# Optimization experiments

Measured on AMD Instinct MI355X. Metric: run time of the kernel, lower is better.

The kernel has to match this reference:

```python
import jax, jax.numpy as jnp
import numpy as np
from jax import lax

T, B, A_DIM, Z_DIM, K_MIX, HID = 128, 256, 16, 32, 8, 128
Q_REG = 1e-3
R_REG = 1e-3


def setup_inputs() -> dict:
    key = jax.random.key(0)
    ks = jax.random.split(key, 16)
    s = 1.0 / np.sqrt(HID)
    reg = 0.9
    as_ = jax.random.normal(ks[0], (T, B, A_DIM), dtype=jnp.float32)
    mat_A_K = (1.0 - reg) * jax.random.normal(ks[1], (K_MIX, Z_DIM, Z_DIM)) + reg * jnp.eye(Z_DIM)
    mat_C_K = (1.0 - reg) * jax.random.normal(ks[2], (K_MIX, A_DIM, Z_DIM)) + reg * jnp.eye(A_DIM, Z_DIM)
    # Cholesky factors of near-identity SPD matrices (as in torch init)
    Q_L = jnp.tril(0.05 * jax.random.normal(ks[3], (Z_DIM, Z_DIM))) + jnp.eye(Z_DIM)
    R_L = jnp.tril(0.05 * jax.random.normal(ks[4], (A_DIM, A_DIM))) + jnp.eye(A_DIM)
    init_mean = jnp.zeros((Z_DIM,), dtype=jnp.float32)
    init_cov = jnp.eye(Z_DIM, dtype=jnp.float32)
    u = lambda k, shp: jax.random.uniform(k, shp, minval=-s, maxval=s, dtype=jnp.float32)
    return dict(
        as_=as_, mat_A_K=mat_A_K, mat_C_K=mat_C_K, Q_L=Q_L, R_L=R_L,
        init_mean=init_mean, init_cov=init_cov,
        W_ih0=u(ks[5], (4 * HID, A_DIM)), W_hh0=u(ks[6], (4 * HID, HID)),
        b_ih0=u(ks[7], (4 * HID,)), b_hh0=u(ks[8], (4 * HID,)),
        W_ih1=u(ks[9], (4 * HID, HID)), W_hh1=u(ks[10], (4 * HID, HID)),
        b_ih1=u(ks[11], (4 * HID,)), b_hh1=u(ks[12], (4 * HID,)),
        W_out=u(ks[13], (K_MIX, HID)), b_out=u(ks[14], (K_MIX,)),
    )


def _lstm_cell(x, h, c, W_ih, W_hh, b_ih, b_hh):
    g = x @ W_ih.T + b_ih + h @ W_hh.T + b_hh
    i, f, gg, o = jnp.split(g, 4, axis=-1)
    c2 = jax.nn.sigmoid(f) * c + jax.nn.sigmoid(i) * jnp.tanh(gg)
    h2 = jax.nn.sigmoid(o) * jnp.tanh(c2)
    return h2, c2


def reference(as_, mat_A_K, mat_C_K, Q_L, R_L, init_mean, init_cov,
              W_ih0, W_hh0, b_ih0, b_hh0, W_ih1, W_hh1, b_ih1, b_hh1,
              W_out, b_out):
    Tn, Bn, a_dim = as_.shape
    Kn, z_dim, _ = mat_A_K.shape
    Hn = W_hh0.shape[1]
    Q = Q_L @ Q_L.T + Q_REG * jnp.eye(z_dim, dtype=as_.dtype)
    R = R_L @ R_L.T + R_REG * jnp.eye(a_dim, dtype=as_.dtype)

    def weight_model(a, h0, c0, h1, c1):
        h0, c0 = _lstm_cell(a, h0, c0, W_ih0, W_hh0, b_ih0, b_hh0)
        h1, c1 = _lstm_cell(h0, h1, c1, W_ih1, W_hh1, b_ih1, b_hh1)
        w = jax.nn.softmax(h1 @ W_out.T + b_out, axis=-1)
        return w, h0, c0, h1, c1

    def step(carry, a_t):
        mean_p, cov_p, weight, h0, c0, h1, c1 = carry
        # mixture matrices for this step (weight == previous step's w_next; ones at t=0)
        mat_A = jnp.einsum('bk,kij->bij', weight, mat_A_K)
        mat_C = jnp.einsum('bk,kij->bij', weight, mat_C_K)
        # sample_control = ('mean','mean'), observation_mask=None -> a = as_[t]
        w_next, h0, c0, h1, c1 = weight_model(a_t, h0, c0, h1, c1)
        mat_A_next = jnp.einsum('bk,kij->bij', w_next, mat_A_K)
        CP = mat_C @ cov_p                                   # (B,a,z)
        S = CP @ jnp.swapaxes(mat_C, 1, 2) + R               # (B,a,a)
        K_t = cov_p @ jnp.swapaxes(mat_C, 1, 2) @ jnp.linalg.inv(S)
        mean_t = mean_p + K_t @ (a_t[..., None] - mat_C @ mean_p)
        mean_p2 = mat_A_next @ mean_t
        cov_t = cov_p - K_t @ CP
        cov_t = 0.5 * (cov_t + jnp.swapaxes(cov_t, 1, 2))
        cov_p2 = mat_A_next @ cov_t @ jnp.swapaxes(mat_A_next, 1, 2) + Q
        cov_p2 = 0.5 * (cov_p2 + jnp.swapaxes(cov_p2, 1, 2))
        new_carry = (mean_p2, cov_p2, w_next, h0, c0, h1, c1)
        outs = (mean_t, cov_t, mean_p2, cov_p2, mat_A, mat_C, a_t)
        return new_carry, outs

    init = (
        jnp.broadcast_to(init_mean[None, :, None], (Bn, z_dim, 1)),
        jnp.broadcast_to(init_cov[None], (Bn, z_dim, z_dim)),
        jnp.ones((Bn, Kn), dtype=as_.dtype),
        jnp.zeros((Bn, Hn), dtype=as_.dtype), jnp.zeros((Bn, Hn), dtype=as_.dtype),
        jnp.zeros((Bn, Hn), dtype=as_.dtype), jnp.zeros((Bn, Hn), dtype=as_.dtype),
    )
    carry, ys = lax.scan(step, init, as_)
    means, covs, next_means, next_covs, mat_As, mat_Cs, a_seq = ys
    w_fin = carry[2]
    mat_A_fin = jnp.einsum('bk,kij->bij', w_fin, mat_A_K)
    mat_C_fin = jnp.einsum('bk,kij->bij', w_fin, mat_C_K)
    mat_As = jnp.concatenate([mat_As, mat_A_fin[None]], axis=0)   # (T+1,B,z,z)
    mat_Cs = jnp.concatenate([mat_Cs, mat_C_fin[None]], axis=0)   # (T+1,B,a,z)
    a_out = a_seq[:, None]                                        # (T,1,B,a) as in torch stack
    return means, covs, next_means, next_covs, mat_As, mat_Cs, a_out
```

## Files before the change

### kernel.cpp

```cpp
#include <hip/hip_runtime.h>
#include <hip/hip_fp16.h>
#include <math.h>

#define T_STEPS 128
#define B_SZ 256
#define AD 16
#define ZD 32
#define KM 8
#define HID 128
#define G4H 512
#define NTHR 512

#define WS_WQ   0
#define WS_WI0  98304
#define WS_BS0  102400
#define WS_BS1  102912
#define WS_Q    103424
#define WS_R    104448

typedef float f32x4 __attribute__((ext_vector_type(4)));

__device__ __forceinline__ unsigned pk16(float lo, float hi) {
  unsigned a = __half_as_ushort(__float2half_rn(lo));
  unsigned b = __half_as_ushort(__float2half_rn(hi));
  return a | (b << 16);
}

__global__ void ssm_prep_kernel(const float* __restrict__ Wih0, const float* __restrict__ Whh0,
                                const float* __restrict__ Wih1, const float* __restrict__ Whh1,
                                const float* __restrict__ bih0, const float* __restrict__ bhh0,
                                const float* __restrict__ bih1, const float* __restrict__ bhh1,
                                const float* __restrict__ QL, const float* __restrict__ RL,
                                float* __restrict__ ws) {
  unsigned* wsu = (unsigned*)ws;
  int tid = blockIdx.x * blockDim.x + threadIdx.x;
  int nt = gridDim.x * blockDim.x;
  for (int j = tid; j < G4H; j += nt) {
    for (int d4 = 0; d4 < 48; ++d4) {
      for (int m = 0; m < 4; ++m) {
        int dd = (d4 & 15) * 4 + m;
        const float* src = (d4 < 16) ? Whh0 : (d4 < 32) ? Wih1 : Whh1;
        wsu[WS_WQ + (d4 * 512 + j) * 4 + m] =
            pk16(src[j * 128 + 2 * dd], src[j * 128 + 2 * dd + 1]);
      }
    }
    for (int k = 0; k < 8; ++k)
      wsu[WS_WI0 + k * 512 + j] = pk16(Wih0[j * 16 + 2 * k], Wih0[j * 16 + 2 * k + 1]);
    ws[WS_BS0 + j] = bih0[j] + bhh0[j];
    ws[WS_BS1 + j] = bih1[j] + bhh1[j];
  }
  for (int e = tid; e < ZD * ZD; e += nt) {
    int i = e >> 5, j = e & 31;
    float s = 0.f;
    for (int k = 0; k < ZD; ++k) s += QL[i * ZD + k] * QL[j * ZD + k];
    if (i == j) s += 0.001f;
    ws[WS_Q + e] = s;
  }
  for (int e = tid; e < AD * AD; e += nt) {
    int i = e >> 4, j = e & 15;
    float s = 0.f;
    for (int k = 0; k < AD; ++k) s += RL[i * AD + k] * RL[j * AD + k];
    if (i == j) s += 0.001f;
    ws[WS_R + e] = s;
  }
}

__device__ __forceinline__ float sigm(float x) { return 1.0f / (1.0f + expf(-x)); }
__device__ __forceinline__ float dotv(f32x4 a, f32x4 b) {
  return a[0] * b[0] + a[1] * b[1] + a[2] * b[2] + a[3] * b[3];
}
__device__ __forceinline__ void st_nt(float* p, float v) { __builtin_nontemporal_store(v, p); }
__device__ __forceinline__ void st_nt4(float* p, f32x4 v) {
  __builtin_nontemporal_store(v, (f32x4*)p);
}

__device__ __forceinline__ float dot2f(unsigned a, unsigned b, float c) {
#if __has_builtin(__builtin_amdgcn_fdot2)
  typedef _Float16 h2 __attribute__((ext_vector_type(2)));
  union U { unsigned u; h2 h; };
  U ua, ub; ua.u = a; ub.u = b;
  return __builtin_amdgcn_fdot2(ua.h, ub.h, c, false);
#else
  union U { unsigned u; _Float16 h[2]; };
  U ua, ub; ua.u = a; ub.u = b;
  return c + (float)ua.h[0] * (float)ub.h[0] + (float)ua.h[1] * (float)ub.h[1];
#endif
}

struct alignas(16) LS {
  unsigned ap[8];
  unsigned h0p[64];
  unsigned h1p[64];
  float g[G4H];
  float lgp[16];
};

__global__ void __launch_bounds__(NTHR, 2) ssm_lstm_kernel(
    const float* __restrict__ as_, const float* __restrict__ AK, const float* __restrict__ CK,
    const float* __restrict__ Wout, const float* __restrict__ bout,
    const float* __restrict__ ws, float* __restrict__ out) {
  __shared__ LS s;
  const int tid = threadIdx.x;
  const int b = blockIdx.x;
  const unsigned* wsu = (const unsigned*)ws;
  const uint4* Wg = (const uint4*)(wsu + WS_WQ);
  const f32x4* AK4 = (const f32x4*)AK;
  const f32x4* CK4 = (const f32x4*)CK;

  float* o_As = out + (size_t)T_STEPS * B_SZ * ZD + (size_t)T_STEPS * B_SZ * ZD * ZD +
                (size_t)T_STEPS * B_SZ * ZD + (size_t)T_STEPS * B_SZ * ZD * ZD;
  float* o_Cs = o_As + (size_t)(T_STEPS + 1) * B_SZ * ZD * ZD;
  float* o_a = o_Cs + (size_t)(T_STEPS + 1) * B_SZ * AD * ZD;

  const uint4* h0p4 = (const uint4*)s.h0p;
  const uint4* h1p4 = (const uint4*)s.h1p;
  const uint4* ap4 = (const uint4*)s.ap;

  unsigned wi0r[8];
  #pragma unroll
  for (int k = 0; k < 8; ++k) wi0r[k] = wsu[WS_WI0 + k * 512 + tid];
  const float bs0r = ws[WS_BS0 + tid];
  const float bs1r = ws[WS_BS1 + tid];
  float woutr[8];
  #pragma unroll
  for (int gi = 0; gi < KM; ++gi) woutr[gi] = (tid < HID) ? Wout[gi * HID + tid] : 0.f;
  float boutr[8];
  #pragma unroll
  for (int k = 0; k < KM; ++k) boutr[k] = bout[k];

  float c0r = 0.f, c1r = 0.f;

  if (tid < 64) { s.h0p[tid] = 0u; s.h1p[tid] = 0u; }
  if (tid < AD) {
    float v = as_[(size_t)b * AD + tid];
    ((__half*)s.ap)[tid] = __float2half_rn(v);
    st_nt(&o_a[(size_t)b * AD + tid], v);
  }
  if (tid < 256) {
    f32x4 acc = {0.f, 0.f, 0.f, 0.f};
    #pragma unroll
    for (int k = 0; k < KM; ++k) acc += AK4[k * 256 + tid];
    st_nt4(&o_As[(size_t)b * 1024 + tid * 4], acc);
  } else if (tid < 384) {
    int idx = tid - 256;
    f32x4 acc = {0.f, 0.f, 0.f, 0.f};
    #pragma unroll
    for (int k = 0; k < KM; ++k) acc += CK4[k * 128 + idx];
    st_nt4(&o_Cs[(size_t)b * 512 + idx * 4], acc);
  }
  __syncthreads();

  for (int t = 0; t < T_STEPS; ++t) {
    const size_t tb2 = (size_t)(t + 1) * B_SZ + b;

    {
      float acc = bs0r;
      #pragma unroll
      for (int k4 = 0; k4 < 2; ++k4) {
        uint4 av = ap4[k4];
        acc = dot2f(av.x, wi0r[k4 * 4 + 0], acc);
        acc = dot2f(av.y, wi0r[k4 * 4 + 1], acc);
        acc = dot2f(av.z, wi0r[k4 * 4 + 2], acc);
        acc = dot2f(av.w, wi0r[k4 * 4 + 3], acc);
      }
      #pragma unroll
      for (int d4 = 0; d4 < 16; ++d4) {
        uint4 w = Wg[d4 * 512 + tid];
        uint4 hv = h0p4[d4];
        acc = dot2f(hv.x, w.x, acc);
        acc = dot2f(hv.y, w.y, acc);
        acc = dot2f(hv.z, w.z, acc);
        acc = dot2f(hv.w, w.w, acc);
      }
      s.g[tid] = acc;
    }
    __syncthreads();

    if (tid < HID) {
      float ig = sigm(s.g[tid]);
      float fg = sigm(s.g[HID + tid]);
      float gg = tanhf(s.g[2 * HID + tid]);
      float og = sigm(s.g[3 * HID + tid]);
      c0r = fg * c0r + ig * gg;
      ((__half*)s.h0p)[tid] = __float2half_rn(og * tanhf(c0r));
    }
    __syncthreads();

    {
      float acc = bs1r;
      #pragma unroll
      for (int d4 = 0; d4 < 16; ++d4) {
        uint4 w = Wg[(16 + d4) * 512 + tid];
        uint4 hv = h0p4[d4];
        acc = dot2f(hv.x, w.x, acc);
        acc = dot2f(hv.y, w.y, acc);
        acc = dot2f(hv.z, w.z, acc);
        acc = dot2f(hv.w, w.w, acc);
      }
      #pragma unroll
      for (int d4 = 0; d4 < 16; ++d4) {
        uint4 w = Wg[(32 + d4) * 512 + tid];
        uint4 hv = h1p4[d4];
        acc = dot2f(hv.x, w.x, acc);
        acc = dot2f(hv.y, w.y, acc);
        acc = dot2f(hv.z, w.z, acc);
        acc = dot2f(hv.w, w.w, acc);
      }
      s.g[tid] = acc;
    }
    __syncthreads();

    if (tid < HID) {
      float ig = sigm(s.g[tid]);
      float fg = sigm(s.g[HID + tid]);
      float gg = tanhf(s.g[2 * HID + tid]);
      float og = sigm(s.g[3 * HID + tid]);
      c1r = fg * c1r + ig * gg;
      float h1u = og * tanhf(c1r);
      ((__half*)s.h1p)[tid] = __float2half_rn(h1u);
      int w2 = tid >> 6, lane = tid & 63;
      #pragma unroll
      for (int gi = 0; gi < KM; ++gi) {
        float p = woutr[gi] * h1u;
        #pragma unroll
        for (int m = 32; m >= 1; m >>= 1) p += __shfl_xor(p, m);
        if (lane == 0) s.lgp[w2 * KM + gi] = p;
      }
    }
    __syncthreads();

    {
      float lg[KM];
      float mx = -1e30f;
      #pragma unroll
      for (int k = 0; k < KM; ++k) {
        lg[k] = s.lgp[k] + s.lgp[KM + k] + boutr[k];
        mx = fmaxf(mx, lg[k]);
      }
      float sum = 0.f;
      #pragma unroll
      for (int k = 0; k < KM; ++k) { lg[k] = expf(lg[k] - mx); sum += lg[k]; }
      float inv = 1.0f / sum;
      #pragma unroll
      for (int k = 0; k < KM; ++k) lg[k] *= inv;
      if (tid < 256) {
        f32x4 acc = {0.f, 0.f, 0.f, 0.f};
        #pragma unroll
        for (int k = 0; k < KM; ++k) acc += lg[k] * AK4[k * 256 + tid];
        st_nt4(&o_As[tb2 * 1024 + tid * 4], acc);
      } else if (tid < 384) {
        int idx = tid - 256;
        f32x4 acc = {0.f, 0.f, 0.f, 0.f};
        #pragma unroll
        for (int k = 0; k < KM; ++k) acc += lg[k] * CK4[k * 128 + idx];
        st_nt4(&o_Cs[tb2 * 512 + idx * 4], acc);
      } else if (tid >= 448 && tid < 448 + AD && t < T_STEPS - 1) {
        int i = tid - 448;
        float v = as_[tb2 * AD + i];
        ((__half*)s.ap)[i] = __float2half_rn(v);
        st_nt(&o_a[tb2 * AD + i], v);
      }
    }
    __syncthreads();
  }
}

struct alignas(16) KS {
  float P[ZD * 36];
  float An[ZD * 36];
  float Mt[ZD * 36];
  float MtT[ZD * 36];
  float Sy[ZD * 36];
  float ACt[ZD * 36];
  float Qs[ZD * 36];
  float C[AD * 36];
  float Aug[AD * 52];
  float Kk[ZD * 20];
  float Rs[AD * AD];
  float meanp[ZD], meant[ZD], r[AD], af[AD];
};

__global__ void __launch_bounds__(256, 1) ssm_kalman_kernel(
    const float* __restrict__ as_, const float* __restrict__ initm,
    const float* __restrict__ initc, const float* __restrict__ ws,
    float* __restrict__ out) {
  __shared__ KS s;
  const int l = threadIdx.x;
  const int b = blockIdx.x;
  const int i32 = l & 31, cq = l >> 5;
  const int i16 = l & 15, j16 = l >> 4;

  float* o_means = out;
  float* o_covs = o_means + (size_t)T_STEPS * B_SZ * ZD;
  float* o_nmean = o_covs + (size_t)T_STEPS * B_SZ * ZD * ZD;
  float* o_ncovs = o_nmean + (size_t)T_STEPS * B_SZ * ZD;
  const float* o_As = o_ncovs + (size_t)T_STEPS * B_SZ * ZD * ZD;
  const float* o_Cs = o_As + (size_t)(T_STEPS + 1) * B_SZ * ZD * ZD;

  f32x4* P4 = (f32x4*)s.P;
  f32x4* An4 = (f32x4*)s.An;
  f32x4* Mt4 = (f32x4*)s.Mt;
  f32x4* MtT4 = (f32x4*)s.MtT;
  f32x4* Sy4 = (f32x4*)s.Sy;
  f32x4* ACt4 = (f32x4*)s.ACt;
  f32x4* Q4 = (f32x4*)s.Qs;
  f32x4* C4 = (f32x4*)s.C;
  f32x4* Aug4 = (f32x4*)s.Aug;
  f32x4* Kk4 = (f32x4*)s.Kk;
  f32x4* af4 = (f32x4*)s.af;
  const f32x4* r4 = (const f32x4*)s.r;
  const f32x4* meanp4 = (const f32x4*)s.meanp;
  const f32x4* meant4 = (const f32x4*)s.meant;

  #pragma unroll
  for (int q = 0; q < 4; ++q) {
    int e = q * 256 + l;
    s.P[(e >> 5) * 36 + (e & 31)] = initc[e];
    s.Qs[(e >> 5) * 36 + (e & 31)] = ws[WS_Q + e];
  }
  s.Rs[l] = ws[WS_R + l];
  if (l < ZD) s.meanp[l] = initm[l];
  {
    const f32x4* gc = (const f32x4*)&o_Cs[(size_t)b * 512];
    if (l < 128) C4[(l >> 3) * 9 + (l & 7)] = gc[l];
    const f32x4* ga = (const f32x4*)&o_As[((size_t)B_SZ + b) * 1024];
    An4[(l >> 3) * 9 + (l & 7)] = ga[l];
    if (l < 4) af4[l] = ((const f32x4*)&as_[(size_t)b * AD])[l];
  }
  __syncthreads();

  for (int t = 0; t < T_STEPS; ++t) {
    const size_t tb = (size_t)t * B_SZ + b;
    const bool pf = (t < T_STEPS - 1);

    f32x4 pfC = {0, 0, 0, 0};
    f32x4 pfA = {0, 0, 0, 0};
    f32x4 pfa = {0, 0, 0, 0};
    if (pf) {
      if (l >= 128) pfC = ((const f32x4*)&o_Cs[(tb + B_SZ) * 512])[l - 128];
      pfA = ((const f32x4*)&o_As[(tb + 2 * B_SZ) * 1024])[l];
      if (l < 4) pfa = ((const f32x4*)&as_[(tb + B_SZ) * AD])[l];
    }

    {
      float a0 = 0.f, a1 = 0.f;
      #pragma unroll
      for (int k4 = 0; k4 < 8; ++k4) {
        f32x4 cr = C4[i16 * 9 + k4];
        a0 += dotv(cr, P4[j16 * 9 + k4]);
        a1 += dotv(cr, P4[(j16 + 16) * 9 + k4]);
      }
      s.Aug[i16 * 52 + AD + j16] = a0;
      s.Aug[i16 * 52 + AD + j16 + 16] = a1;
    }
    __syncthreads();

    {
      float acc = s.Rs[i16 * AD + j16];
      #pragma unroll
      for (int k4 = 0; k4 < 8; ++k4)
        acc += dotv(Aug4[i16 * 13 + 4 + k4], C4[j16 * 9 + k4]);
      s.Aug[i16 * 52 + j16] = acc;
      if (l >= 240) {
        int ii = l - 240;
        float rr = s.af[ii];
        #pragma unroll
        for (int k4 = 0; k4 < 8; ++k4) rr -= dotv(C4[ii * 9 + k4], meanp4[k4]);
        s.r[ii] = rr;
      }
    }
    __syncthreads();

    if (l < 64) {
      const int lc = (l < 48) ? l : 47;
      float col[16];
      #pragma unroll
      for (int i = 0; i < AD; ++i) col[i] = s.Aug[i * 52 + lc];
      #pragma unroll
      for (int j = 0; j < AD; ++j) {
        float pd = __shfl(col[j], j);
        float pinv = 1.0f / pd;
        float oldj = col[j];
        #pragma unroll
        for (int i = 0; i < AD; ++i) {
          if (i == j) continue;
          float fi = __shfl(col[i], j);
          col[i] = fmaf(-(fi * pinv), oldj, col[i]);
        }
        col[j] = oldj * pinv;
      }
      if (l >= AD && l < AD + ZD) {
        int rr = l - AD;
        f32x4 v0 = {col[0], col[1], col[2], col[3]};
        f32x4 v1 = {col[4], col[5], col[6], col[7]};
        f32x4 v2 = {col[8], col[9], col[10], col[11]};
        f32x4 v3 = {col[12], col[13], col[14], col[15]};
        Kk4[rr * 5 + 0] = v0;
        Kk4[rr * 5 + 1] = v1;
        Kk4[rr * 5 + 2] = v2;
        Kk4[rr * 5 + 3] = v3;
      }
    } else if (pf && l >= 128) {
      int idx = l - 128;
      C4[(idx >> 3) * 9 + (idx & 7)] = pfC;
    }
    __syncthreads();

    {
      f32x4 acc = {0.f, 0.f, 0.f, 0.f};
      #pragma unroll
      for (int k4 = 0; k4 < 4; ++k4) {
        f32x4 kv = Kk4[i32 * 5 + k4];
        #pragma unroll
        for (int kk = 0; kk < 4; ++kk) {
          f32x4 cpk = Aug4[(4 * k4 + kk) * 13 + 4 + cq];
          acc += kv[kk] * cpk;
        }
      }
      f32x4 mv = P4[i32 * 9 + cq] - acc;
      Mt4[i32 * 9 + cq] = mv;
      #pragma unroll
      for (int jj = 0; jj < 4; ++jj) s.MtT[(4 * cq + jj) * 36 + i32] = mv[jj];
    }
    __syncthreads();

    {
      f32x4 sv = 0.5f * (Mt4[i32 * 9 + cq] + MtT4[i32 * 9 + cq]);
      Sy4[i32 * 9 + cq] = sv;
      st_nt4(&o_covs[tb * 1024 + i32 * 32 + cq * 4], sv);
      if (l < ZD) {
        float acc = s.meanp[l];
        #pragma unroll
        for (int m = 0; m < 4; ++m) acc += dotv(Kk4[l * 5 + m], r4[m]);
        s.meant[l] = acc;
        st_nt(&o_means[tb * ZD + l], acc);
      }
    }
    __syncthreads();

    {
      float c0 = 0.f, c1 = 0.f, c2 = 0.f, c3 = 0.f;
      #pragma unroll
      for (int k4 = 0; k4 < 8; ++k4) {
        f32x4 an = An4[i32 * 9 + k4];
        c0 += dotv(an, Sy4[(4 * cq + 0) * 9 + k4]);
        c1 += dotv(an, Sy4[(4 * cq + 1) * 9 + k4]);
        c2 += dotv(an, Sy4[(4 * cq + 2) * 9 + k4]);
        c3 += dotv(an, Sy4[(4 * cq + 3) * 9 + k4]);
      }
      f32x4 v = {c0, c1, c2, c3};
      ACt4[i32 * 9 + cq] = v;
    }
    __syncthreads();

    {
      if (l < ZD) {
        float acc = 0.f;
        #pragma unroll
        for (int k4 = 0; k4 < 8; ++k4) acc += dotv(An4[l * 9 + k4], meant4[k4]);
        s.meanp[l] = acc;
        st_nt(&o_nmean[tb * ZD + l], acc);
      }
      float c0 = 0.f, c1 = 0.f, c2 = 0.f, c3 = 0.f;
      #pragma unroll
      for (int k4 = 0; k4 < 8; ++k4) {
        f32x4 ac = ACt4[i32 * 9 + k4];
        c0 += dotv(ac, An4[(4 * cq + 0) * 9 + k4]);
        c1 += dotv(ac, An4[(4 * cq + 1) * 9 + k4]);
        c2 += dotv(ac, An4[(4 * cq + 2) * 9 + k4]);
        c3 += dotv(ac, An4[(4 * cq + 3) * 9 + k4]);
      }
      f32x4 mv = {c0, c1, c2, c3};
      Mt4[i32 * 9 + cq] = mv;
      #pragma unroll
      for (int jj = 0; jj < 4; ++jj) s.MtT[(4 * cq + jj) * 36 + i32] = mv[jj];
    }
    __syncthreads();

    {
      f32x4 pv = 0.5f * (Mt4[i32 * 9 + cq] + MtT4[i32 * 9 + cq]) + Q4[i32 * 9 + cq];
      P4[i32 * 9 + cq] = pv;
      st_nt4(&o_ncovs[tb * 1024 + i32 * 32 + cq * 4], pv);
    }
    __syncthreads();

    if (pf) {
      An4[(l >> 3) * 9 + (l & 7)] = pfA;
      if (l < 4) af4[l] = pfa;
    }
    __syncthreads();
  }
}

extern "C" void kernel_launch(void* const* d_in, const int* in_sizes, int n_in,
                              void* d_out, int out_size, void* d_ws, size_t ws_size,
                              hipStream_t stream) {
  const float* as_ = (const float*)d_in[0];
  const float* AK = (const float*)d_in[1];
  const float* CK = (const float*)d_in[2];
  const float* QL = (const float*)d_in[3];
  const float* RL = (const float*)d_in[4];
  const float* initm = (const float*)d_in[5];
  const float* initc = (const float*)d_in[6];
  const float* Wih0 = (const float*)d_in[7];
  const float* Whh0 = (const float*)d_in[8];
  const float* bih0 = (const float*)d_in[9];
  const float* bhh0 = (const float*)d_in[10];
  const float* Wih1 = (const float*)d_in[11];
  const float* Whh1 = (const float*)d_in[12];
  const float* bih1 = (const float*)d_in[13];
  const float* bhh1 = (const float*)d_in[14];
  const float* Wout = (const float*)d_in[15];
  const float* bout = (const float*)d_in[16];
  float* ws = (float*)d_ws;
  float* out = (float*)d_out;

  ssm_prep_kernel<<<16, 256, 0, stream>>>(Wih0, Whh0, Wih1, Whh1, bih0, bhh0, bih1, bhh1,
                                          QL, RL, ws);
  ssm_lstm_kernel<<<B_SZ, NTHR, 0, stream>>>(as_, AK, CK, Wout, bout, ws, out);
  ssm_kalman_kernel<<<B_SZ, 256, 0, stream>>>(as_, initm, initc, ws, out);
}
```

Measured before the change: 1.588 ms.

## Fuse LSTM and Kalman kernels into one warp-specialized pipelined kernel

Merges the LSTM weight-model kernel and the Kalman filter kernel into a single block per batch element. Threads 0-255 run the Kalman recursion and threads 256-511 run the LSTM, each LSTM thread computing two gates. Per-step A and C matrices pass through shared-memory ring buffers with a two-step lag, so the Kalman side no longer re-reads As/Cs from global memory. The aim is to remove the separate kernel launch and the global round trip and to overlap the two recurrences. In exchange the block uses more shared memory, both halves share the same barriers, and the LSTM now runs on half as many threads.

Measured after the change: 5.766 ms. 3.63x slower.

```diff
diff --git a/kernel.cpp b/kernel.cpp
--- a/kernel.cpp
+++ b/kernel.cpp
@@ -9,7 +9,6 @@
 #define KM 8
 #define HID 128
 #define G4H 512
-#define NTHR 512
 
 #define WS_WQ   0
 #define WS_WI0  98304
@@ -87,7 +86,19 @@
 #endif
 }
 
-struct alignas(16) LS {
+struct alignas(16) FS {
+  float P[ZD * 36];
+  float Mt[ZD * 36];
+  float Sy[ZD * 36];
+  float ACt[ZD * 36];
+  float Qs[ZD * 36];
+  float Aug[AD * 52];
+  float Kk[ZD * 20];
+  float Rs[AD * AD];
+  float meanp[ZD], meant[ZD], r[AD];
+  float Cring[4][AD * 36];
+  float Aring[4][ZD * 36];
+  float afr[4][AD];
   unsigned ap[8];
   unsigned h0p[64];
   unsigned h1p[64];
@@ -95,398 +106,382 @@
   float lgp[16];
 };
 
-__global__ void __launch_bounds__(NTHR, 2) ssm_lstm_kernel(
+__global__ void __launch_bounds__(512, 2) ssm_fused_kernel(
     const float* __restrict__ as_, const float* __restrict__ AK, const float* __restrict__ CK,
     const float* __restrict__ Wout, const float* __restrict__ bout,
+    const float* __restrict__ initm, const float* __restrict__ initc,
     const float* __restrict__ ws, float* __restrict__ out) {
-  __shared__ LS s;
+  __shared__ FS s;
   const int tid = threadIdx.x;
   const int b = blockIdx.x;
+  const bool isK = (tid < 256);
+  const int kl = tid;
+  const int lt = tid - 256;
   const unsigned* wsu = (const unsigned*)ws;
-  const uint4* Wg = (const uint4*)(wsu + WS_WQ);
-  const f32x4* AK4 = (const f32x4*)AK;
-  const f32x4* CK4 = (const f32x4*)CK;
-
-  float* o_As = out + (size_t)T_STEPS * B_SZ * ZD + (size_t)T_STEPS * B_SZ * ZD * ZD +
-                (size_t)T_STEPS * B_SZ * ZD + (size_t)T_STEPS * B_SZ * ZD * ZD;
-  float* o_Cs = o_As + (size_t)(T_STEPS + 1) * B_SZ * ZD * ZD;
-  float* o_a = o_Cs + (size_t)(T_STEPS + 1) * B_SZ * AD * ZD;
-
-  const uint4* h0p4 = (const uint4*)s.h0p;
-  const uint4* h1p4 = (const uint4*)s.h1p;
-  const uint4* ap4 = (const uint4*)s.ap;
-
-  unsigned wi0r[8];
-  #pragma unroll
-  for (int k = 0; k < 8; ++k) wi0r[k] = wsu[WS_WI0 + k * 512 + tid];
-  const float bs0r = ws[WS_BS0 + tid];
-  const float bs1r = ws[WS_BS1 + tid];
-  float woutr[8];
-  #pragma unroll
-  for (int gi = 0; gi < KM; ++gi) woutr[gi] = (tid < HID) ? Wout[gi * HID + tid] : 0.f;
-  float boutr[8];
-  #pragma unroll
-  for (int k = 0; k < KM; ++k) boutr[k] = bout[k];
-
-  float c0r = 0.f, c1r = 0.f;
-
-  if (tid < 64) { s.h0p[tid] = 0u; s.h1p[tid] = 0u; }
-  if (tid < AD) {
-    float v = as_[(size_t)b * AD + tid];
-    ((__half*)s.ap)[tid] = __float2half_rn(v);
-    st_nt(&o_a[(size_t)b * AD + tid], v);
-  }
-  if (tid < 256) {
-    f32x4 acc = {0.f, 0.f, 0.f, 0.f};
-    #pragma unroll
-    for (int k = 0; k < KM; ++k) acc += AK4[k * 256 + tid];
-    st_nt4(&o_As[(size_t)b * 1024 + tid * 4], acc);
-  } else if (tid < 384) {
-    int idx = tid - 256;
-    f32x4 acc = {0.f, 0.f, 0.f, 0.f};
-    #pragma unroll
-    for (int k = 0; k < KM; ++k) acc += CK4[k * 128 + idx];
-    st_nt4(&o_Cs[(size_t)b * 512 + idx * 4], acc);
-  }
-  __syncthreads();
-
-  for (int t = 0; t < T_STEPS; ++t) {
-    const size_t tb2 = (size_t)(t + 1) * B_SZ + b;
-
-    {
-      float acc = bs0r;
-      #pragma unroll
-      for (int k4 = 0; k4 < 2; ++k4) {
-        uint4 av = ap4[k4];
-        acc = dot2f(av.x, wi0r[k4 * 4 + 0], acc);
-        acc = dot2f(av.y, wi0r[k4 * 4 + 1], acc);
-        acc = dot2f(av.z, wi0r[k4 * 4 + 2], acc);
-        acc = dot2f(av.w, wi0r[k4 * 4 + 3], acc);
-      }
-      #pragma unroll
-      for (int d4 = 0; d4 < 16; ++d4) {
-        uint4 w = Wg[d4 * 512 + tid];
-        uint4 hv = h0p4[d4];
-        acc = dot2f(hv.x, w.x, acc);
-        acc = dot2f(hv.y, w.y, acc);
-        acc = dot2f(hv.z, w.z, acc);
-        acc = dot2f(hv.w, w.w, acc);
-      }
-      s.g[tid] = acc;
-    }
-    __syncthreads();
-
-    if (tid < HID) {
-      float ig = sigm(s.g[tid]);
-      float fg = sigm(s.g[HID + tid]);
-      float gg = tanhf(s.g[2 * HID + tid]);
-      float og = sigm(s.g[3 * HID + tid]);
-      c0r = fg * c0r + ig * gg;
-      ((__half*)s.h0p)[tid] = __float2half_rn(og * tanhf(c0r));
-    }
-    __syncthreads();
-
-    {
-      float acc = bs1r;
-      #pragma unroll
-      for (int d4 = 0; d4 < 16; ++d4) {
-        uint4 w = Wg[(16 + d4) * 512 + tid];
-        uint4 hv = h0p4[d4];
-        acc = dot2f(hv.x, w.x, acc);
-        acc = dot2f(hv.y, w.y, acc);
-        acc = dot2f(hv.z, w.z, acc);
-        acc = dot2f(hv.w, w.w, acc);
-      }
-      #pragma unroll
-      for (int d4 = 0; d4 < 16; ++d4) {
-        uint4 w = Wg[(32 + d4) * 512 + tid];
-        uint4 hv = h1p4[d4];
-        acc = dot2f(hv.x, w.x, acc);
-        acc = dot2f(hv.y, w.y, acc);
-        acc = dot2f(hv.z, w.z, acc);
-        acc = dot2f(hv.w, w.w, acc);
-      }
-      s.g[tid] = acc;
-    }
-    __syncthreads();
-
-    if (tid < HID) {
-      float ig = sigm(s.g[tid]);
-      float fg = sigm(s.g[HID + tid]);
-      float gg = tanhf(s.g[2 * HID + tid]);
-      float og = sigm(s.g[3 * HID + tid]);
-      c1r = fg * c1r + ig * gg;
-      float h1u = og * tanhf(c1r);
-      ((__half*)s.h1p)[tid] = __float2half_rn(h1u);
-      int w2 = tid >> 6, lane = tid & 63;
-      #pragma unroll
-      for (int gi = 0; gi < KM; ++gi) {
-        float p = woutr[gi] * h1u;
-        #pragma unroll
-        for (int m = 32; m >= 1; m >>= 1) p += __shfl_xor(p, m);
-        if (lane == 0) s.lgp[w2 * KM + gi] = p;
-      }
-    }
-    __syncthreads();
-
-    {
-      float lg[KM];
-      float mx = -1e30f;
-      #pragma unroll
-      for (int k = 0; k < KM; ++k) {
-        lg[k] = s.lgp[k] + s.lgp[KM + k] + boutr[k];
-        mx = fmaxf(mx, lg[k]);
-      }
-      float sum = 0.f;
-      #pragma unroll
-      for (int k = 0; k < KM; ++k) { lg[k] = expf(lg[k] - mx); sum += lg[k]; }
-      float inv = 1.0f / sum;
-      #pragma unroll
-      for (int k = 0; k < KM; ++k) lg[k] *= inv;
-      if (tid < 256) {
-        f32x4 acc = {0.f, 0.f, 0.f, 0.f};
-        #pragma unroll
-        for (int k = 0; k < KM; ++k) acc += lg[k] * AK4[k * 256 + tid];
-        st_nt4(&o_As[tb2 * 1024 + tid * 4], acc);
-      } else if (tid < 384) {
-        int idx = tid - 256;
-        f32x4 acc = {0.f, 0.f, 0.f, 0.f};
-        #pragma unroll
-        for (int k = 0; k < KM; ++k) acc += lg[k] * CK4[k * 128 + idx];
-        st_nt4(&o_Cs[tb2 * 512 + idx * 4], acc);
-      } else if (tid >= 448 && tid < 448 + AD && t < T_STEPS - 1) {
-        int i = tid - 448;
-        float v = as_[tb2 * AD + i];
-        ((__half*)s.ap)[i] = __float2half_rn(v);
-        st_nt(&o_a[tb2 * AD + i], v);
-      }
-    }
-    __syncthreads();
-  }
-}
-
-struct alignas(16) KS {
-  float P[ZD * 36];
-  float An[ZD * 36];
-  float Mt[ZD * 36];
-  float MtT[ZD * 36];
-  float Sy[ZD * 36];
-  float ACt[ZD * 36];
-  float Qs[ZD * 36];
-  float C[AD * 36];
-  float Aug[AD * 52];
-  float Kk[ZD * 20];
-  float Rs[AD * AD];
-  float meanp[ZD], meant[ZD], r[AD], af[AD];
-};
-
-__global__ void __launch_bounds__(256, 1) ssm_kalman_kernel(
-    const float* __restrict__ as_, const float* __restrict__ initm,
-    const float* __restrict__ initc, const float* __restrict__ ws,
-    float* __restrict__ out) {
-  __shared__ KS s;
-  const int l = threadIdx.x;
-  const int b = blockIdx.x;
-  const int i32 = l & 31, cq = l >> 5;
-  const int i16 = l & 15, j16 = l >> 4;
 
   float* o_means = out;
   float* o_covs = o_means + (size_t)T_STEPS * B_SZ * ZD;
   float* o_nmean = o_covs + (size_t)T_STEPS * B_SZ * ZD * ZD;
   float* o_ncovs = o_nmean + (size_t)T_STEPS * B_SZ * ZD;
-  const float* o_As = o_ncovs + (size_t)T_STEPS * B_SZ * ZD * ZD;
-  const float* o_Cs = o_As + (size_t)(T_STEPS + 1) * B_SZ * ZD * ZD;
+  float* o_As = o_ncovs + (size_t)T_STEPS * B_SZ * ZD * ZD;
+  float* o_Cs = o_As + (size_t)(T_STEPS + 1) * B_SZ * ZD * ZD;
+  float* o_a = o_Cs + (size_t)(T_STEPS + 1) * B_SZ * AD * ZD;
 
   f32x4* P4 = (f32x4*)s.P;
-  f32x4* An4 = (f32x4*)s.An;
   f32x4* Mt4 = (f32x4*)s.Mt;
-  f32x4* MtT4 = (f32x4*)s.MtT;
   f32x4* Sy4 = (f32x4*)s.Sy;
   f32x4* ACt4 = (f32x4*)s.ACt;
   f32x4* Q4 = (f32x4*)s.Qs;
-  f32x4* C4 = (f32x4*)s.C;
   f32x4* Aug4 = (f32x4*)s.Aug;
   f32x4* Kk4 = (f32x4*)s.Kk;
-  f32x4* af4 = (f32x4*)s.af;
   const f32x4* r4 = (const f32x4*)s.r;
   const f32x4* meanp4 = (const f32x4*)s.meanp;
   const f32x4* meant4 = (const f32x4*)s.meant;
-
-  #pragma unroll
-  for (int q = 0; q < 4; ++q) {
-    int e = q * 256 + l;
-    s.P[(e >> 5) * 36 + (e & 31)] = initc[e];
-    s.Qs[(e >> 5) * 36 + (e & 31)] = ws[WS_Q + e];
-  }
-  s.Rs[l] = ws[WS_R + l];
-  if (l < ZD) s.meanp[l] = initm[l];
-  {
-    const f32x4* gc = (const f32x4*)&o_Cs[(size_t)b * 512];
-    if (l < 128) C4[(l >> 3) * 9 + (l & 7)] = gc[l];
-    const f32x4* ga = (const f32x4*)&o_As[((size_t)B_SZ + b) * 1024];
-    An4[(l >> 3) * 9 + (l & 7)] = ga[l];
-    if (l < 4) af4[l] = ((const f32x4*)&as_[(size_t)b * AD])[l];
+  const uint4* h0p4 = (const uint4*)s.h0p;
+  const uint4* h1p4 = (const uint4*)s.h1p;
+  const uint4* ap4 = (const uint4*)s.ap;
+  const uint4* Wg = (const uint4*)(wsu + WS_WQ);
+  const f32x4* AK4 = (const f32x4*)AK;
+  const f32x4* CK4 = (const f32x4*)CK;
+
+  const int i32 = kl & 31, cq = (kl & 255) >> 5;
+  const int i16 = kl & 15, j16 = (kl & 255) >> 4;
+
+  unsigned wi0rA[8], wi0rB[8];
+  float bs0rA = 0.f, bs0rB = 0.f, bs1rA = 0.f, bs1rB = 0.f;
+  float woutr[8], boutr[8];
+  float c0r = 0.f, c1r = 0.f;
+  float ga = 0.f, gb = 0.f;
+
+  if (!isK) {
+    #pragma unroll
+    for (int k = 0; k < 8; ++k) {
+      wi0rA[k] = wsu[WS_WI0 + k * 512 + lt];
+      wi0rB[k] = wsu[WS_WI0 + k * 512 + lt + 256];
+    }
+    bs0rA = ws[WS_BS0 + lt];
+    bs0rB = ws[WS_BS0 + lt + 256];
+    bs1rA = ws[WS_BS1 + lt];
+    bs1rB = ws[WS_BS1 + lt + 256];
+    #pragma unroll
+    for (int gi = 0; gi < KM; ++gi) woutr[gi] = (lt < HID) ? Wout[gi * HID + lt] : 0.f;
+    #pragma unroll
+    for (int k = 0; k < KM; ++k) boutr[k] = bout[k];
+    if (lt < 128) {
+      f32x4 acc = {0.f, 0.f, 0.f, 0.f};
+      #pragma unroll
+      for (int k = 0; k < KM; ++k) acc += CK4[k * 128 + lt];
+      ((f32x4*)s.Cring[0])[(lt >> 3) * 9 + (lt & 7)] = acc;
+      st_nt4(&o_Cs[(size_t)b * 512 + lt * 4], acc);
+    }
+    {
+      f32x4 acc = {0.f, 0.f, 0.f, 0.f};
+      #pragma unroll
+      for (int k = 0; k < KM; ++k) acc += AK4[k * 256 + lt];
+      st_nt4(&o_As[(size_t)b * 1024 + lt * 4], acc);
+    }
+    if (lt >= 240) {
+      int i2 = lt - 240;
+      float v = as_[(size_t)b * AD + i2];
+      s.afr[0][i2] = v;
+      ((__half*)s.ap)[i2] = __float2half_rn(v);
+      st_nt(&o_a[(size_t)b * AD + i2], v);
+    }
+    if (lt < 64) { s.h0p[lt] = 0u; s.h1p[lt] = 0u; }
+  } else {
+    #pragma unroll
+    for (int q = 0; q < 4; ++q) {
+      int e = q * 256 + kl;
+      s.P[(e >> 5) * 36 + (e & 31)] = initc[e];
+      s.Qs[(e >> 5) * 36 + (e & 31)] = ws[WS_Q + e];
+    }
+    s.Rs[kl] = ws[WS_R + kl];
+    if (kl < ZD) s.meanp[kl] = initm[kl];
   }
   __syncthreads();
 
-  for (int t = 0; t < T_STEPS; ++t) {
-    const size_t tb = (size_t)t * B_SZ + b;
-    const bool pf = (t < T_STEPS - 1);
-
-    f32x4 pfC = {0, 0, 0, 0};
-    f32x4 pfA = {0, 0, 0, 0};
-    f32x4 pfa = {0, 0, 0, 0};
-    if (pf) {
-      if (l >= 128) pfC = ((const f32x4*)&o_Cs[(tb + B_SZ) * 512])[l - 128];
-      pfA = ((const f32x4*)&o_As[(tb + 2 * B_SZ) * 1024])[l];
-      if (l < 4) pfa = ((const f32x4*)&as_[(tb + B_SZ) * AD])[l];
-    }
-
-    {
-      float a0 = 0.f, a1 = 0.f;
-      #pragma unroll
-      for (int k4 = 0; k4 < 8; ++k4) {
-        f32x4 cr = C4[i16 * 9 + k4];
-        a0 += dotv(cr, P4[j16 * 9 + k4]);
-        a1 += dotv(cr, P4[(j16 + 16) * 9 + k4]);
-      }
-      s.Aug[i16 * 52 + AD + j16] = a0;
-      s.Aug[i16 * 52 + AD + j16 + 16] = a1;
-    }
-    __syncthreads();
-
-    {
-      float acc = s.Rs[i16 * AD + j16];
-      #pragma unroll
-      for (int k4 = 0; k4 < 8; ++k4)
-        acc += dotv(Aug4[i16 * 13 + 4 + k4], C4[j16 * 9 + k4]);
-      s.Aug[i16 * 52 + j16] = acc;
-      if (l >= 240) {
-        int ii = l - 240;
-        float rr = s.af[ii];
-        #pragma unroll
-        for (int k4 = 0; k4 < 8; ++k4) rr -= dotv(C4[ii * 9 + k4], meanp4[k4]);
-        s.r[ii] = rr;
-      }
-    }
-    __syncthreads();
-
-    if (l < 64) {
-      const int lc = (l < 48) ? l : 47;
-      float col[16];
-      #pragma unroll
-      for (int i = 0; i < AD; ++i) col[i] = s.Aug[i * 52 + lc];
-      #pragma unroll
-      for (int j = 0; j < AD; ++j) {
-        float pd = __shfl(col[j], j);
-        float pinv = 1.0f / pd;
-        float oldj = col[j];
-        #pragma unroll
-        for (int i = 0; i < AD; ++i) {
-          if (i == j) continue;
-          float fi = __shfl(col[i], j);
-          col[i] = fmaf(-(fi * pinv), oldj, col[i]);
-        }
-        col[j] = oldj * pinv;
-      }
-      if (l >= AD && l < AD + ZD) {
-        int rr = l - AD;
-        f32x4 v0 = {col[0], col[1], col[2], col[3]};
-        f32x4 v1 = {col[4], col[5], col[6], col[7]};
-        f32x4 v2 = {col[8], col[9], col[10], col[11]};
-        f32x4 v3 = {col[12], col[13], col[14], col[15]};
-        Kk4[rr * 5 + 0] = v0;
-        Kk4[rr * 5 + 1] = v1;
-        Kk4[rr * 5 + 2] = v2;
-        Kk4[rr * 5 + 3] = v3;
-      }
-    } else if (pf && l >= 128) {
-      int idx = l - 128;
-      C4[(idx >> 3) * 9 + (idx & 7)] = pfC;
-    }
-    __syncthreads();
-
-    {
-      f32x4 acc = {0.f, 0.f, 0.f, 0.f};
-      #pragma unroll
-      for (int k4 = 0; k4 < 4; ++k4) {
-        f32x4 kv = Kk4[i32 * 5 + k4];
-        #pragma unroll
-        for (int kk = 0; kk < 4; ++kk) {
-          f32x4 cpk = Aug4[(4 * k4 + kk) * 13 + 4 + cq];
-          acc += kv[kk] * cpk;
-        }
-      }
-      f32x4 mv = P4[i32 * 9 + cq] - acc;
-      Mt4[i32 * 9 + cq] = mv;
-      #pragma unroll
-      for (int jj = 0; jj < 4; ++jj) s.MtT[(4 * cq + jj) * 36 + i32] = mv[jj];
-    }
-    __syncthreads();
-
-    {
-      f32x4 sv = 0.5f * (Mt4[i32 * 9 + cq] + MtT4[i32 * 9 + cq]);
-      Sy4[i32 * 9 + cq] = sv;
-      st_nt4(&o_covs[tb * 1024 + i32 * 32 + cq * 4], sv);
-      if (l < ZD) {
-        float acc = s.meanp[l];
-        #pragma unroll
-        for (int m = 0; m < 4; ++m) acc += dotv(Kk4[l * 5 + m], r4[m]);
-        s.meant[l] = acc;
-        st_nt(&o_means[tb * ZD + l], acc);
-      }
-    }
-    __syncthreads();
-
-    {
-      float c0 = 0.f, c1 = 0.f, c2 = 0.f, c3 = 0.f;
-      #pragma unroll
-      for (int k4 = 0; k4 < 8; ++k4) {
-        f32x4 an = An4[i32 * 9 + k4];
-        c0 += dotv(an, Sy4[(4 * cq + 0) * 9 + k4]);
-        c1 += dotv(an, Sy4[(4 * cq + 1) * 9 + k4]);
-        c2 += dotv(an, Sy4[(4 * cq + 2) * 9 + k4]);
-        c3 += dotv(an, Sy4[(4 * cq + 3) * 9 + k4]);
-      }
-      f32x4 v = {c0, c1, c2, c3};
-      ACt4[i32 * 9 + cq] = v;
-    }
-    __syncthreads();
-
-    {
-      if (l < ZD) {
-        float acc = 0.f;
-        #pragma unroll
-        for (int k4 = 0; k4 < 8; ++k4) acc += dotv(An4[l * 9 + k4], meant4[k4]);
-        s.meanp[l] = acc;
-        st_nt(&o_nmean[tb * ZD + l], acc);
-      }
-      float c0 = 0.f, c1 = 0.f, c2 = 0.f, c3 = 0.f;
-      #pragma unroll
-      for (int k4 = 0; k4 < 8; ++k4) {
-        f32x4 ac = ACt4[i32 * 9 + k4];
-        c0 += dotv(ac, An4[(4 * cq + 0) * 9 + k4]);
-        c1 += dotv(ac, An4[(4 * cq + 1) * 9 + k4]);
-        c2 += dotv(ac, An4[(4 * cq + 2) * 9 + k4]);
-        c3 += dotv(ac, An4[(4 * cq + 3) * 9 + k4]);
-      }
-      f32x4 mv = {c0, c1, c2, c3};
-      Mt4[i32 * 9 + cq] = mv;
-      #pragma unroll
-      for (int jj = 0; jj < 4; ++jj) s.MtT[(4 * cq + jj) * 36 + i32] = mv[jj];
-    }
-    __syncthreads();
-
-    {
-      f32x4 pv = 0.5f * (Mt4[i32 * 9 + cq] + MtT4[i32 * 9 + cq]) + Q4[i32 * 9 + cq];
+  for (int i = 0; i < T_STEPS + 2; ++i) {
+    const bool lact = (i < T_STEPS);
+    const bool kact = (i >= 2);
+    const int t = i - 2;
+    const size_t tb = (size_t)(t < 0 ? 0 : t) * B_SZ + b;
+    const size_t tb2 = (size_t)(i + 1) * B_SZ + b;
+    const f32x4* Cc = (const f32x4*)s.Cring[t & 3];
+    const f32x4* Ac = (const f32x4*)s.Aring[(t + 1) & 3];
+
+    if (isK) {
+      if (kact) {
+        float a0 = 0.f, a1 = 0.f;
+        #pragma unroll
+        for (int k4 = 0; k4 < 8; ++k4) {
+          f32x4 cr = Cc[i16 * 9 + k4];
+          a0 += dotv(cr, P4[j16 * 9 + k4]);
+          a1 += dotv(cr, P4[(j16 + 16) * 9 + k4]);
+        }
+        s.Aug[i16 * 52 + AD + j16] = a0;
+        s.Aug[i16 * 52 + AD + j16 + 16] = a1;
+      }
+    } else if (lact) {
+      ga = bs0rA;
+      gb = bs0rB;
+      #pragma unroll
+      for (int k4 = 0; k4 < 2; ++k4) {
+        uint4 av = ap4[k4];
+        ga = dot2f(av.x, wi0rA[k4 * 4 + 0], ga);
+        ga = dot2f(av.y, wi0rA[k4 * 4 + 1], ga);
+        ga = dot2f(av.z, wi0rA[k4 * 4 + 2], ga);
+        ga = dot2f(av.w, wi0rA[k4 * 4 + 3], ga);
+        gb = dot2f(av.x, wi0rB[k4 * 4 + 0], gb);
+        gb = dot2f(av.y, wi0rB[k4 * 4 + 1], gb);
+        gb = dot2f(av.z, wi0rB[k4 * 4 + 2], gb);
+        gb = dot2f(av.w, wi0rB[k4 * 4 + 3], gb);
+      }
+      #pragma unroll
+      for (int d4 = 0; d4 < 8; ++d4) {
+        uint4 hv = h0p4[d4];
+        uint4 wA = Wg[d4 * 512 + lt];
+        uint4 wB = Wg[d4 * 512 + lt + 256];
+        ga = dot2f(hv.x, wA.x, ga); ga = dot2f(hv.y, wA.y, ga);
+        ga = dot2f(hv.z, wA.z, ga); ga = dot2f(hv.w, wA.w, ga);
+        gb = dot2f(hv.x, wB.x, gb); gb = dot2f(hv.y, wB.y, gb);
+        gb = dot2f(hv.z, wB.z, gb); gb = dot2f(hv.w, wB.w, gb);
+      }
+    }
+    __syncthreads();
+
+    if (isK) {
+      if (kact) {
+        float b0 = s.Rs[i16 * AD + j16];
+        #pragma unroll
+        for (int k4 = 0; k4 < 8; ++k4)
+          b0 += dotv(Aug4[i16 * 13 + 4 + k4], Cc[j16 * 9 + k4]);
+        s.Aug[i16 * 52 + j16] = b0;
+        if (kl >= 240) {
+          int ii = kl - 240;
+          float rr = s.afr[t & 3][ii];
+          #pragma unroll
+          for (int k4 = 0; k4 < 8; ++k4) rr -= dotv(Cc[ii * 9 + k4], meanp4[k4]);
+          s.r[ii] = rr;
+        }
+      }
+    } else if (lact) {
+      #pragma unroll
+      for (int d4 = 8; d4 < 16; ++d4) {
+        uint4 hv = h0p4[d4];
+        uint4 wA = Wg[d4 * 512 + lt];
+        uint4 wB = Wg[d4 * 512 + lt + 256];
+        ga = dot2f(hv.x, wA.x, ga); ga = dot2f(hv.y, wA.y, ga);
+        ga = dot2f(hv.z, wA.z, ga); ga = dot2f(hv.w, wA.w, ga);
+        gb = dot2f(hv.x, wB.x, gb); gb = dot2f(hv.y, wB.y, gb);
+        gb = dot2f(hv.z, wB.z, gb); gb = dot2f(hv.w, wB.w, gb);
+      }
+      s.g[lt] = ga;
+      s.g[lt + 256] = gb;
+    }
+    __syncthreads();
+
+    if (isK) {
+      if (kact && kl < 64) {
+        const int lc = (kl < 48) ? kl : 47;
+        float col[16];
+        #pragma unroll
+        for (int q = 0; q < AD; ++q) col[q] = s.Aug[q * 52 + lc];
+        #pragma unroll
+        for (int j = 0; j < AD; ++j) {
+          float pd = __shfl(col[j], j);
+          float pinv = 1.0f / pd;
+          float oldj = col[j];
+          #pragma unroll
+          for (int q = 0; q < AD; ++q) {
+            if (q == j) continue;
+            float fi = __shfl(col[q], j);
+            col[q] = fmaf(-(fi * pinv), oldj, col[q]);
+          }
+          col[j] = oldj * pinv;
+        }
+        if (kl >= AD && kl < AD + ZD) {
+          int rr = kl - AD;
+          f32x4 v0 = {col[0], col[1], col[2], col[3]};
+          f32x4 v1 = {col[4], col[5], col[6], col[7]};
+          f32x4 v2 = {col[8], col[9], col[10], col[11]};
+          f32x4 v3 = {col[12], col[13], col[14], col[15]};
+          Kk4[rr * 5 + 0] = v0;
+          Kk4[rr * 5 + 1] = v1;
+          Kk4[rr * 5 + 2] = v2;
+          Kk4[rr * 5 + 3] = v3;
+        }
+      }
+    } else if (lact && lt < HID) {
+      float ig = sigm(s.g[lt]);
+      float fg = sigm(s.g[HID + lt]);
+      float gg = tanhf(s.g[2 * HID + lt]);
+      float og = sigm(s.g[3 * HID + lt]);
+      c0r = fg * c0r + ig * gg;
+      ((__half*)s.h0p)[lt] = __float2half_rn(og * tanhf(c0r));
+    }
+    __syncthreads();
+
+    if (isK) {
+      if (kact) {
+        if (kl < ZD) {
+          float acc = s.meanp[kl];
+          #pragma unroll
+          for (int m = 0; m < 4; ++m) acc += dotv(Kk4[kl * 5 + m], r4[m]);
+          s.meant[kl] = acc;
+          st_nt(&o_means[tb * ZD + kl], acc);
+        }
+        f32x4 acc = {0.f, 0.f, 0.f, 0.f};
+        #pragma unroll
+        for (int k4 = 0; k4 < 4; ++k4) {
+          f32x4 kv = Kk4[i32 * 5 + k4];
+          #pragma unroll
+          for (int kk = 0; kk < 4; ++kk)
+            acc += kv[kk] * Aug4[(4 * k4 + kk) * 13 + 4 + cq];
+        }
+        Mt4[i32 * 9 + cq] = P4[i32 * 9 + cq] - acc;
+      }
+    } else if (lact) {
+      ga = bs1rA;
+      gb = bs1rB;
+      #pragma unroll
+      for (int d4 = 0; d4 < 16; ++d4) {
+        uint4 hv = h0p4[d4];
+        uint4 wA = Wg[(16 + d4) * 512 + lt];
+        uint4 wB = Wg[(16 + d4) * 512 + lt + 256];
+        ga = dot2f(hv.x, wA.x, ga); ga = dot2f(hv.y, wA.y, ga);
+        ga = dot2f(hv.z, wA.z, ga); ga = dot2f(hv.w, wA.w, ga);
+        gb = dot2f(hv.x, wB.x, gb); gb = dot2f(hv.y, wB.y, gb);
+        gb = dot2f(hv.z, wB.z, gb); gb = dot2f(hv.w, wB.w, gb);
+      }
+    }
+    __syncthreads();
+
+    if (isK) {
+      if (kact) {
+        f32x4 mv = Mt4[i32 * 9 + cq];
+        f32x4 sv;
+        #pragma unroll
+        for (int jj = 0; jj < 4; ++jj)
+          sv[jj] = 0.5f * (mv[jj] + s.Mt[(4 * cq + jj) * 36 + i32]);
+        Sy4[i32 * 9 + cq] = sv;
+        st_nt4(&o_covs[tb * 1024 + i32 * 32 + cq * 4], sv);
+      }
+    } else if (lact) {
+      #pragma unroll
+      for (int d4 = 0; d4 < 16; ++d4) {
+        uint4 hv = h1p4[d4];
+        uint4 wA = Wg[(32 + d4) * 512 + lt];
+        uint4 wB = Wg[(32 + d4) * 512 + lt + 256];
+        ga = dot2f(hv.x, wA.x, ga); ga = dot2f(hv.y, wA.y, ga);
+        ga = dot2f(hv.z, wA.z, ga); ga = dot2f(hv.w, wA.w, ga);
+        gb = dot2f(hv.x, wB.x, gb); gb = dot2f(hv.y, wB.y, gb);
+        gb = dot2f(hv.z, wB.z, gb); gb = dot2f(hv.w, wB.w, gb);
+      }
+      s.g[lt] = ga;
+      s.g[lt + 256] = gb;
+    }
+    __syncthreads();
+
+    if (isK) {
+      if (kact) {
+        float c0 = 0.f, c1 = 0.f, c2 = 0.f, c3 = 0.f;
+        #pragma unroll
+        for (int k4 = 0; k4 < 8; ++k4) {
+          f32x4 an = Ac[i32 * 9 + k4];
+          c0 += dotv(an, Sy4[(4 * cq + 0) * 9 + k4]);
+          c1 += dotv(an, Sy4[(4 * cq + 1) * 9 + k4]);
+          c2 += dotv(an, Sy4[(4 * cq + 2) * 9 + k4]);
+          c3 += dotv(an, Sy4[(4 * cq + 3) * 9 + k4]);
+        }
+        f32x4 v = {c0, c1, c2, c3};
+        ACt4[i32 * 9 + cq] = v;
+      }
+    } else if (lact && lt < HID) {
+      float ig = sigm(s.g[lt]);
+      float fg = sigm(s.g[HID + lt]);
+      float gg = tanhf(s.g[2 * HID + lt]);
+      float og = sigm(s.g[3 * HID + lt]);
+      c1r = fg * c1r + ig * gg;
+      float h1u = og * tanhf(c1r);
+      ((__half*)s.h1p)[lt] = __float2half_rn(h1u);
+      int w2 = lt >> 6, lane = lt & 63;
+      #pragma unroll
+      for (int gi = 0; gi < KM; ++gi) {
+        float p = woutr[gi] * h1u;
+        #pragma unroll
+        for (int m = 32; m >= 1; m >>= 1) p += __shfl_xor(p, m);
+        if (lane == 0) s.lgp[w2 * KM + gi] = p;
+      }
+    }
+    __syncthreads();
+
+    if (isK) {
+      if (kact) {
+        if (kl < ZD) {
+          float acc = 0.f;
+          #pragma unroll
+          for (int k4 = 0; k4 < 8; ++k4) acc += dotv(Ac[kl * 9 + k4], meant4[k4]);
+          s.meanp[kl] = acc;
+          st_nt(&o_nmean[tb * ZD + kl], acc);
+        }
+        float c0 = 0.f, c1 = 0.f, c2 = 0.f, c3 = 0.f;
+        #pragma unroll
+        for (int k4 = 0; k4 < 8; ++k4) {
+          f32x4 ac = ACt4[i32 * 9 + k4];
+          c0 += dotv(ac, Ac[(4 * cq + 0) * 9 + k4]);
+          c1 += dotv(ac, Ac[(4 * cq + 1) * 9 + k4]);
+          c2 += dotv(ac, Ac[(4 * cq + 2) * 9 + k4]);
+          c3 += dotv(ac, Ac[(4 * cq + 3) * 9 + k4]);
+        }
+        f32x4 mv = {c0, c1, c2, c3};
+        Mt4[i32 * 9 + cq] = mv;
+      }
+    } else if (lact) {
+      float lg[KM];
+      float mx = -1e30f;
+      #pragma unroll
+      for (int k = 0; k < KM; ++k) {
+        lg[k] = s.lgp[k] + s.lgp[KM + k] + boutr[k];
+        mx = fmaxf(mx, lg[k]);
+      }
+      float sum = 0.f;
+      #pragma unroll
+      for (int k = 0; k < KM; ++k) { lg[k] = expf(lg[k] - mx); sum += lg[k]; }
+      float inv = 1.0f / sum;
+      #pragma unroll
+      for (int k = 0; k < KM; ++k) lg[k] *= inv;
+      {
+        f32x4 acc = {0.f, 0.f, 0.f, 0.f};
+        #pragma unroll
+        for (int k = 0; k < KM; ++k) acc += lg[k] * AK4[k * 256 + lt];
+        ((f32x4*)s.Aring[(i + 1) & 3])[(lt >> 3) * 9 + (lt & 7)] = acc;
+        st_nt4(&o_As[tb2 * 1024 + lt * 4], acc);
+      }
+      if (lt < 128) {
+        f32x4 acc = {0.f, 0.f, 0.f, 0.f};
+        #pragma unroll
+        for (int k = 0; k < KM; ++k) acc += lg[k] * CK4[k * 128 + lt];
+        ((f32x4*)s.Cring[(i + 1) & 3])[(lt >> 3) * 9 + (lt & 7)] = acc;
+        st_nt4(&o_Cs[tb2 * 512 + lt * 4], acc);
+      } else if (lt >= 240 && i + 1 < T_STEPS) {
+        int i2 = lt - 240;
+        float v = as_[tb2 * AD + i2];
+        s.afr[(i + 1) & 3][i2] = v;
+        ((__half*)s.ap)[i2] = __float2half_rn(v);
+        st_nt(&o_a[tb2 * AD + i2], v);
+      }
+    }
+    __syncthreads();
+
+    if (isK && kact) {
+      f32x4 mv = Mt4[i32 * 9 + cq];
+      f32x4 pv;
+      #pragma unroll
+      for (int jj = 0; jj < 4; ++jj)
+        pv[jj] = 0.5f * (mv[jj] + s.Mt[(4 * cq + jj) * 36 + i32]);
+      pv += Q4[i32 * 9 + cq];
       P4[i32 * 9 + cq] = pv;
       st_nt4(&o_ncovs[tb * 1024 + i32 * 32 + cq * 4], pv);
-    }
-    __syncthreads();
-
-    if (pf) {
-      An4[(l >> 3) * 9 + (l & 7)] = pfA;
-      if (l < 4) af4[l] = pfa;
     }
     __syncthreads();
   }
@@ -517,6 +512,5 @@
 
   ssm_prep_kernel<<<16, 256, 0, stream>>>(Wih0, Whh0, Wih1, Whh1, bih0, bhh0, bih1, bhh1,
                                           QL, RL, ws);
-  ssm_lstm_kernel<<<B_SZ, NTHR, 0, stream>>>(as_, AK, CK, Wout, bout, ws, out);
-  ssm_kalman_kernel<<<B_SZ, 256, 0, stream>>>(as_, initm, initc, ws, out);
-}
+  ssm_fused_kernel<<<B_SZ, 512, 0, stream>>>(as_, AK, CK, Wout, bout, initm, initc, ws, out);
+}
```
